# Performance work log

Hardware: AMD Instinct MI355X
Metric: run time of the kernel (lower is better)

## Reference

```python
import jax, jax.numpy as jnp
import numpy as np

B, S, H, SSZ, IN = 1024, 100, 128, 100, 2


def _gru(x, h, Wih, Whh, bih, bhh):
    # PyTorch GRU cell: gates ordered (reset, update, new)
    gx = x @ Wih.T + bih
    gh = h @ Whh.T + bhh
    xr, xz, xn = jnp.split(gx, 3, axis=-1)
    hr, hz, hn = jnp.split(gh, 3, axis=-1)
    r = jax.nn.sigmoid(xr + hr)
    z = jax.nn.sigmoid(xz + hz)
    n = jnp.tanh(xn + r * hn)
    return (1.0 - z) * n + z * h


def _attn(inst_h, rnn_out, W, v):
    # inst_h: [B,S,H], rnn_out: [B,H] -> softmax attention weights [B,S]
    h = jnp.concatenate([inst_h, jnp.broadcast_to(rnn_out[:, None, :], inst_h.shape)], axis=-1)
    s = jax.nn.relu(jnp.einsum('bsk,kh->bsh', h, W)) @ v
    return jax.nn.softmax(s, axis=1)


def setup_inputs() -> dict:
    key = jax.random.key(0)
    k = jax.random.split(key, 32)
    p = lambda i, shape, sc=0.05: sc * jax.random.normal(k[i], shape, jnp.float32)
    instance = jax.random.uniform(k[0], (B, S, IN), jnp.float32)
    # solutions must be per-row permutations of node indices
    solution_1 = jnp.argsort(jax.random.uniform(k[1], (B, S)), axis=1).astype(jnp.int32)
    solution_2 = jnp.argsort(jax.random.uniform(k[2], (B, S)), axis=1).astype(jnp.int32)
    eps = jax.random.normal(k[3], (B, SSZ), jnp.float32)
    return dict(
        instance=instance, solution_1=solution_1, solution_2=solution_2, eps=eps,
        emb_i_W=p(4, (H, IN)), emb_i_b=jnp.zeros(H, jnp.float32),
        emb_r_W=p(5, (H, IN)), emb_r_b=jnp.zeros(H, jnp.float32),
        attn_W=p(6, (2 * H, H)), attn_v=p(7, (H,)),
        gru_Wih=p(8, (3 * H, H)), gru_Whh=p(9, (3 * H, H)),
        gru_bih=jnp.zeros(3 * H, jnp.float32), gru_bhh=jnp.zeros(3 * H, jnp.float32),
        grud_Wih=p(10, (3 * H, 2 * H)), grud_Whh=p(11, (3 * H, H)),
        grud_bih=jnp.zeros(3 * H, jnp.float32), grud_bhh=jnp.zeros(3 * H, jnp.float32),
        enc_fc1_W=p(12, (SSZ, H)), enc_fc1_b=jnp.zeros(SSZ, jnp.float32),
        enc_fc2_W=p(13, (SSZ, H)), enc_fc2_b=jnp.zeros(SSZ, jnp.float32),
        ptr_W=p(14, (2 * H, H)), ptr_v=p(15, (H,)),
        pfc1_W=p(16, (2 * H, 2 * H + SSZ)), pfc1_b=jnp.zeros(2 * H, jnp.float32),
        pfc2_W=p(17, (H, 2 * H)), pfc2_b=jnp.zeros(H, jnp.float32),
    )


def reference(instance, solution_1, solution_2, eps,
              emb_i_W, emb_i_b, emb_r_W, emb_r_b, attn_W, attn_v,
              gru_Wih, gru_Whh, gru_bih, gru_bhh,
              grud_Wih, grud_Whh, grud_bih, grud_bhh,
              enc_fc1_W, enc_fc1_b, enc_fc2_W, enc_fc2_b,
              ptr_W, ptr_v, pfc1_W, pfc1_b, pfc2_W, pfc2_b):
    b_idx = jnp.arange(B)
    inst_h = instance @ emb_i_W.T + emb_i_b  # [B,S,H]
    emb_r = lambda x: x @ emb_r_W.T + emb_r_b
    take = lambda ptr: instance[b_idx, ptr]  # gather node coords [B,IN]

    # ---------------- Encoder ----------------
    def enc_step(carry, ptr):
        h1, h2, ref_h = carry
        h1 = _gru(ref_h, h1, gru_Wih, gru_Whh, gru_bih, gru_bhh)
        a = _attn(inst_h, h1, attn_W, attn_v)
        context = jnp.einsum('bs,bsh->bh', a, inst_h)
        ref_h = emb_r(take(ptr))
        rnn_in = jnp.concatenate([ref_h, context], axis=-1)  # [B,2H]
        h2 = _gru(rnn_in, h2, grud_Wih, grud_Whh, grud_bih, grud_bhh)
        return (h1, h2, ref_h), None

    z0 = jnp.zeros((B, H), instance.dtype)
    ref_h0 = emb_r(take(solution_1[:, 0]))
    (_, h2, _), _ = jax.lax.scan(enc_step, (z0, z0, ref_h0), solution_1[:, 1:].T)
    mu = h2 @ enc_fc1_W.T + enc_fc1_b
    log_var = h2 @ enc_fc2_W.T + enc_fc2_b
    Z = mu + eps * jnp.exp(0.5 * log_var)

    # ---------------- Decoder (teacher forcing) ----------------
    mask0 = jnp.ones((B, S), instance.dtype).at[b_idx, solution_2[:, 0]].set(0.0)

    def dec_step(carry, ptr):
        h1, ref_in, mask = carry
        ref_h = emb_r(ref_in)
        h1 = _gru(ref_h, h1, gru_Wih, gru_Whh, gru_bih, gru_bhh)
        a = _attn(inst_h, h1, attn_W, attn_v)
        context = jnp.einsum('bs,bsh->bh', a, inst_h)
        fc_in = jnp.concatenate([context, Z, ref_h], axis=-1)  # [B, 2H+SSZ]
        fc_out = (fc_in @ pfc1_W.T + pfc1_b) @ pfc2_W.T + pfc2_b  # no activation, as in torch
        hcat = jnp.concatenate([inst_h, jnp.broadcast_to(fc_out[:, None, :], inst_h.shape)], axis=-1)
        logits = jnp.tanh(jnp.einsum('bsk,kh->bsh', hcat, ptr_W)) @ ptr_v  # [B,S]
        probs = jax.nn.softmax(logits + jnp.log(mask), axis=1)
        logp = jnp.log(probs[b_idx, ptr])
        pred = jnp.argmax(probs, axis=1)
        mask = mask.at[b_idx, ptr].set(0.0)  # tsp.update_mask: mark chosen node visited
        return (h1, take(ptr), mask), (pred, logp)

    init = (z0, take(solution_2[:, 0]), mask0)
    _, (preds, logps) = jax.lax.scan(dec_step, init, solution_2[:, 1:].T)
    tour_idx = jnp.concatenate([solution_2[:, :1], preds.T.astype(solution_2.dtype)], axis=1)
    tour_logp = logps.T  # [B, S-1]
    return (mu, log_var, Z, tour_idx, tour_logp)
```

## Files before the change

### kernel.cpp

```cpp
#include <hip/hip_runtime.h>
#include <math.h>

static constexpr int NB  = 1024;
static constexpr int NS  = 100;
static constexpr int NH  = 128;
static constexpr int GPB = 2;
static constexpr int NTHR = 256;
static constexpr int NBLK = NB / GPB;

static constexpr int OUT_MU = 0;
static constexpr int OUT_LV = NB * NS;
static constexpr int OUT_Z  = 2 * NB * NS;
static constexpr int OUT_TI = 3 * NB * NS;
static constexpr int OUT_LP = 4 * NB * NS;

#define NEGF (-3.4e38f)

template<int C4>
__device__ __forceinline__ void dot2x3f(const float* __restrict__ wr0,
        const float* __restrict__ wr1, const float* __restrict__ wr2,
        const float* __restrict__ x0, const float* __restrict__ x1,
        float& r00, float& r01, float& r10, float& r11, float& r20, float& r21)
{
    const float4* W0 = reinterpret_cast<const float4*>(wr0);
    const float4* W1 = reinterpret_cast<const float4*>(wr1);
    const float4* W2 = reinterpret_cast<const float4*>(wr2);
    const float4* X0 = reinterpret_cast<const float4*>(x0);
    const float4* X1 = reinterpret_cast<const float4*>(x1);
    float a00 = 0.f, a01 = 0.f, a10 = 0.f, a11 = 0.f, a20 = 0.f, a21 = 0.f;
    #pragma unroll 8
    for (int c = 0; c < C4; ++c) {
        float4 u0 = W0[c], u1 = W1[c], u2 = W2[c];
        float4 v0 = X0[c], v1 = X1[c];
        a00 = fmaf(u0.x, v0.x, a00); a00 = fmaf(u0.y, v0.y, a00); a00 = fmaf(u0.z, v0.z, a00); a00 = fmaf(u0.w, v0.w, a00);
        a01 = fmaf(u0.x, v1.x, a01); a01 = fmaf(u0.y, v1.y, a01); a01 = fmaf(u0.z, v1.z, a01); a01 = fmaf(u0.w, v1.w, a01);
        a10 = fmaf(u1.x, v0.x, a10); a10 = fmaf(u1.y, v0.y, a10); a10 = fmaf(u1.z, v0.z, a10); a10 = fmaf(u1.w, v0.w, a10);
        a11 = fmaf(u1.x, v1.x, a11); a11 = fmaf(u1.y, v1.y, a11); a11 = fmaf(u1.z, v1.z, a11); a11 = fmaf(u1.w, v1.w, a11);
        a20 = fmaf(u2.x, v0.x, a20); a20 = fmaf(u2.y, v0.y, a20); a20 = fmaf(u2.z, v0.z, a20); a20 = fmaf(u2.w, v0.w, a20);
        a21 = fmaf(u2.x, v1.x, a21); a21 = fmaf(u2.y, v1.y, a21); a21 = fmaf(u2.z, v1.z, a21); a21 = fmaf(u2.w, v1.w, a21);
    }
    r00 = a00; r01 = a01; r10 = a10; r11 = a11; r20 = a20; r21 = a21;
}

template<int C4>
__device__ __forceinline__ void dot2f(const float* __restrict__ w,
        const float* __restrict__ x0, const float* __restrict__ x1, float& r0, float& r1)
{
    const float4* W = reinterpret_cast<const float4*>(w);
    const float4* X0 = reinterpret_cast<const float4*>(x0);
    const float4* X1 = reinterpret_cast<const float4*>(x1);
    float a0 = 0.f, a1 = 0.f;
    #pragma unroll 8
    for (int c = 0; c < C4; ++c) {
        float4 u = W[c];
        float4 v0 = X0[c], v1 = X1[c];
        a0 = fmaf(u.x, v0.x, a0); a0 = fmaf(u.y, v0.y, a0); a0 = fmaf(u.z, v0.z, a0); a0 = fmaf(u.w, v0.w, a0);
        a1 = fmaf(u.x, v1.x, a1); a1 = fmaf(u.y, v1.y, a1); a1 = fmaf(u.z, v1.z, a1); a1 = fmaf(u.w, v1.w, a1);
    }
    r0 = a0; r1 = a1;
}

template<int C4>
__device__ __forceinline__ void dot1f(const float* __restrict__ w,
        const float* __restrict__ x0, float& r0)
{
    const float4* W = reinterpret_cast<const float4*>(w);
    const float4* X0 = reinterpret_cast<const float4*>(x0);
    float a0 = 0.f;
    #pragma unroll 8
    for (int c = 0; c < C4; ++c) {
        float4 u = W[c];
        float4 v0 = X0[c];
        a0 = fmaf(u.x, v0.x, a0); a0 = fmaf(u.y, v0.y, a0); a0 = fmaf(u.z, v0.z, a0); a0 = fmaf(u.w, v0.w, a0);
    }
    r0 = a0;
}

template<int C4>
__device__ __forceinline__ double dotwd(const float* __restrict__ w, const float* __restrict__ x)
{
    const float4* W = reinterpret_cast<const float4*>(w);
    double a = 0.0;
    #pragma unroll 8
    for (int c = 0; c < C4; ++c) {
        float4 u = W[c];
        const float* p = x + 4 * c;
        a = fma((double)u.x, (double)p[0], a);
        a = fma((double)u.y, (double)p[1], a);
        a = fma((double)u.z, (double)p[2], a);
        a = fma((double)u.w, (double)p[3], a);
    }
    return a;
}

__device__ __forceinline__ void gruc(const float* __restrict__ bih, const float* __restrict__ bhh,
        const float* __restrict__ pa, const float* __restrict__ pb, float* __restrict__ h, int j)
{
    double r = 1.0 / (1.0 + exp(-(((double)pa[j]        + (double)bih[j])        + ((double)pb[j]        + (double)bhh[j]))));
    double z = 1.0 / (1.0 + exp(-(((double)pa[NH + j]   + (double)bih[NH + j])   + ((double)pb[NH + j]   + (double)bhh[NH + j]))));
    double n = tanh(((double)pa[2*NH + j] + (double)bih[2*NH + j]) + r * ((double)pb[2*NH + j] + (double)bhh[2*NH + j]));
    h[j] = (float)((1.0 - z) * n + z * (double)h[j]);
}

__global__ __launch_bounds__(NTHR) void vae_v14(
    const float* __restrict__ instance, const int* __restrict__ sol1,
    const int* __restrict__ sol2, const float* __restrict__ eps,
    const float* __restrict__ emb_i_W, const float* __restrict__ emb_i_b,
    const float* __restrict__ emb_r_W, const float* __restrict__ emb_r_b,
    const float* __restrict__ attn_W, const float* __restrict__ attn_v,
    const float* __restrict__ gru_Wih, const float* __restrict__ gru_Whh,
    const float* __restrict__ gru_bih, const float* __restrict__ gru_bhh,
    const float* __restrict__ grud_Wih, const float* __restrict__ grud_Whh,
    const float* __restrict__ grud_bih, const float* __restrict__ grud_bhh,
    const float* __restrict__ efc1_W, const float* __restrict__ efc1_b,
    const float* __restrict__ efc2_W, const float* __restrict__ efc2_b,
    const float* __restrict__ ptr_W, const float* __restrict__ ptr_v,
    const float* __restrict__ pfc1_W, const float* __restrict__ pfc1_b,
    const float* __restrict__ pfc2_W, const float* __restrict__ pfc2_b,
    float* __restrict__ out)
{
    __shared__ float  s_x[GPB][360];
    __shared__ float  s_h1[GPB][NH], s_h2[GPB][NH], s_fco[GPB][NH];
    __shared__ float  s_fch[GPB][256];
    __shared__ float  s_pa[GPB][3 * NH], s_pb[GPB][3 * NH];
    __shared__ double s_qh[GPB][NH];
    __shared__ double s_qpA[GPB][NH], s_qpB[GPB][NH];
    __shared__ double2 dAa[NH], dAp[NH];
    __shared__ double dAba[NH], dAbp[NH];
    __shared__ float  s_lg[GPB][NS], s_a[GPB][NS];
    __shared__ float  s_c0[GPB][NS], s_c1[GPB][NS], s_msk[GPB][NS];
    __shared__ float  t_wi0[NH], t_wi1[NH], t_bi[NH];
    __shared__ float  t_wr0[NH], t_wr1[NH], t_br[NH];
    __shared__ float  t_va[NH], t_vp[NH];
    __shared__ float  t_gbih[3*NH], t_gbhh[3*NH], t_dbih[3*NH], t_dbhh[3*NH];
    __shared__ float  t_p1b[256], t_p2b[NH];
    __shared__ int    s_sol1[GPB][NS], s_sol2[GPB][NS];
    __shared__ float  s_red[GPB][2];
    __shared__ double s_redd[GPB][2];
    __shared__ int    s_ri[GPB][2];
    __shared__ float  s_rc0[GPB], s_rc1[GPB];

    const int tid = threadIdx.x;
    const int bbase = blockIdx.x * GPB;
    const int j = tid & (NH - 1);
    const int half = tid >> 7;
    const int g = half;
    const int lane = tid & 63;
    const int wid = (tid >> 6) & 1;

    if (tid < NH) {
        t_wi0[tid] = emb_i_W[2*tid]; t_wi1[tid] = emb_i_W[2*tid+1]; t_bi[tid] = emb_i_b[tid];
        t_wr0[tid] = emb_r_W[2*tid]; t_wr1[tid] = emb_r_W[2*tid+1]; t_br[tid] = emb_r_b[tid];
        t_va[tid] = attn_v[tid]; t_vp[tid] = ptr_v[tid];
        t_p2b[tid] = pfc2_b[tid];
    }
    t_p1b[tid] = pfc1_b[tid];
    for (int i = tid; i < 3 * NH; i += NTHR) {
        t_gbih[i] = gru_bih[i]; t_gbhh[i] = gru_bhh[i];
        t_dbih[i] = grud_bih[i]; t_dbhh[i] = grud_bhh[i];
    }
    for (int i = tid; i < GPB * NS; i += NTHR) {
        int gg = i / NS, s = i - gg * NS;
        s_c0[gg][s] = instance[(size_t)((bbase + gg) * NS + s) * 2 + 0];
        s_c1[gg][s] = instance[(size_t)((bbase + gg) * NS + s) * 2 + 1];
        s_sol1[gg][s] = sol1[(bbase + gg) * NS + s];
        s_sol2[gg][s] = sol2[(bbase + gg) * NS + s];
    }
    s_h1[g][j] = 0.f;
    s_h2[g][j] = 0.f;
    __syncthreads();
    {
        const float* Wm = (half == 0) ? attn_W : ptr_W;
        double a0 = 0.0, a1 = 0.0, ab = 0.0;
        for (int k = 0; k < NH; ++k) {
            double wv = (double)Wm[(size_t)k * NH + j];
            a0 = fma((double)t_wi0[k], wv, a0);
            a1 = fma((double)t_wi1[k], wv, a1);
            ab = fma((double)t_bi[k],  wv, ab);
        }
        if (half == 0) { dAa[j].x = a0; dAa[j].y = a1; dAba[j] = ab; }
        else           { dAp[j].x = a0; dAp[j].y = a1; dAbp[j] = ab; }
    }
    {
        int sp = s_sol1[g][0];
        s_x[g][j] = fmaf(s_c0[g][sp], t_wr0[j], fmaf(s_c1[g][sp], t_wr1[j], t_br[j]));
    }
    __syncthreads();

    for (int t = 1; t < NS; ++t) {
        if (half == 0) {
            float a00,a01,a10,a11,a20,a21;
            dot2x3f<32>(gru_Wih + (size_t)j * NH, gru_Wih + (size_t)(NH + j) * NH,
                        gru_Wih + (size_t)(2*NH + j) * NH, s_x[0], s_x[1],
                        a00,a01,a10,a11,a20,a21);
            s_pa[0][j] = a00;        s_pa[1][j] = a01;
            s_pa[0][NH + j] = a10;   s_pa[1][NH + j] = a11;
            s_pa[0][2*NH + j] = a20; s_pa[1][2*NH + j] = a21;
        } else {
            float a00,a01,a10,a11,a20,a21;
            dot2x3f<32>(gru_Whh + (size_t)j * NH, gru_Whh + (size_t)(NH + j) * NH,
                        gru_Whh + (size_t)(2*NH + j) * NH, s_h1[0], s_h1[1],
                        a00,a01,a10,a11,a20,a21);
            s_pb[0][j] = a00;        s_pb[1][j] = a01;
            s_pb[0][NH + j] = a10;   s_pb[1][NH + j] = a11;
            s_pb[0][2*NH + j] = a20; s_pb[1][2*NH + j] = a21;
        }
        __syncthreads();
        gruc(t_gbih, t_gbhh, s_pa[g], s_pb[g], s_h1[g], j);
        __syncthreads();
        {
            const float* col = attn_W + (size_t)NH * NH + j;
            const int k0 = half * 64;
            double a00=0.0,a01=0.0,a02=0.0,a03=0.0;
            double a10=0.0,a11=0.0,a12=0.0,a13=0.0;
            #pragma unroll 8
            for (int k = 0; k < 64; k += 4) {
                float w0 = col[(size_t)(k0+k+0) * NH];
                float w1 = col[(size_t)(k0+k+1) * NH];
                float w2 = col[(size_t)(k0+k+2) * NH];
                float w3 = col[(size_t)(k0+k+3) * NH];
                float4 h0 = *reinterpret_cast<const float4*>(&s_h1[0][k0+k]);
                float4 h1v = *reinterpret_cast<const float4*>(&s_h1[1][k0+k]);
                a00 = fma((double)w0, (double)h0.x, a00);
                a01 = fma((double)w1, (double)h0.y, a01);
                a02 = fma((double)w2, (double)h0.z, a02);
                a03 = fma((double)w3, (double)h0.w, a03);
                a10 = fma((double)w0, (double)h1v.x, a10);
                a11 = fma((double)w1, (double)h1v.y, a11);
                a12 = fma((double)w2, (double)h1v.z, a12);
                a13 = fma((double)w3, (double)h1v.w, a13);
            }
            if (half == 0) { s_qpA[0][j] = (a00+a01)+(a02+a03); s_qpA[1][j] = (a10+a11)+(a12+a13); }
            else           { s_qpB[0][j] = (a00+a01)+(a02+a03); s_qpB[1][j] = (a10+a11)+(a12+a13); }
        }
        __syncthreads();
        s_qh[g][j] = dAba[j] + (s_qpA[g][j] + s_qpB[g][j]);
        __syncthreads();
        if (j < NS) {
            double c00 = (double)s_c0[g][j], c10 = (double)s_c1[g][j];
            double acc0 = 0.0, acc1 = 0.0, acc2 = 0.0, acc3 = 0.0;
            #pragma unroll 4
            for (int h = 0; h < NH; h += 4) {
                double2 A0 = dAa[h+0], A1 = dAa[h+1], A2 = dAa[h+2], A3 = dAa[h+3];
                double p0 = fma(c00, A0.x, fma(c10, A0.y, s_qh[g][h+0]));
                double p1 = fma(c00, A1.x, fma(c10, A1.y, s_qh[g][h+1]));
                double p2 = fma(c00, A2.x, fma(c10, A2.y, s_qh[g][h+2]));
                double p3 = fma(c00, A3.x, fma(c10, A3.y, s_qh[g][h+3]));
                acc0 = fma(fmax(p0, 0.0), (double)t_va[h+0], acc0);
                acc1 = fma(fmax(p1, 0.0), (double)t_va[h+1], acc1);
                acc2 = fma(fmax(p2, 0.0), (double)t_va[h+2], acc2);
                acc3 = fma(fmax(p3, 0.0), (double)t_va[h+3], acc3);
            }
            s_lg[g][j] = (float)(((acc0 + acc1) + (acc2 + acc3)));
        }
        __syncthreads();
        {
            float a = s_lg[g][lane];
            float b = (lane + 64 < NS) ? s_lg[g][lane + 64] : NEGF;
            float m = fmaxf(a, b);
            m = fmaxf(m, __shfl_xor(m, 32)); m = fmaxf(m, __shfl_xor(m, 16));
            m = fmaxf(m, __shfl_xor(m, 8));  m = fmaxf(m, __shfl_xor(m, 4));
            m = fmaxf(m, __shfl_xor(m, 2));  m = fmaxf(m, __shfl_xor(m, 1));
            float fv = 0.f;
            if (j < NS) { fv = (float)exp((double)s_lg[g][j] - (double)m); s_a[g][j] = fv; }
            double ps = (double)fv;
            ps += __shfl_xor(ps, 32); ps += __shfl_xor(ps, 16);
            ps += __shfl_xor(ps, 8);  ps += __shfl_xor(ps, 4);
            ps += __shfl_xor(ps, 2);  ps += __shfl_xor(ps, 1);
            if (lane == 0) s_redd[g][wid] = ps;
        }
        __syncthreads();
        if (j < NS) {
            double se = s_redd[g][0] + s_redd[g][1];
            s_a[g][j] = (float)((double)s_a[g][j] / se);
        }
        __syncthreads();
        {
            float w0 = t_wi0[j], w1 = t_wi1[j], bb = t_bi[j];
            double a0 = 0.0, a1 = 0.0, a2 = 0.0, a3 = 0.0;
            #pragma unroll 5
            for (int s = 0; s < NS; s += 4) {
                float ih0 = fmaf(s_c0[g][s+0], w0, fmaf(s_c1[g][s+0], w1, bb));
                float ih1 = fmaf(s_c0[g][s+1], w0, fmaf(s_c1[g][s+1], w1, bb));
                float ih2 = fmaf(s_c0[g][s+2], w0, fmaf(s_c1[g][s+2], w1, bb));
                float ih3 = fmaf(s_c0[g][s+3], w0, fmaf(s_c1[g][s+3], w1, bb));
                a0 += (double)s_a[g][s+0] * (double)ih0;
                a1 += (double)s_a[g][s+1] * (double)ih1;
                a2 += (double)s_a[g][s+2] * (double)ih2;
                a3 += (double)s_a[g][s+3] * (double)ih3;
            }
            s_x[g][NH + j] = (float)(((a0 + a1) + (a2 + a3)));
            int sp = s_sol1[g][t];
            s_x[g][j] = fmaf(s_c0[g][sp], t_wr0[j], fmaf(s_c1[g][sp], t_wr1[j], t_br[j]));
        }
        __syncthreads();
        if (half == 0) {
            float a00,a01,a10,a11,a20,a21;
            dot2x3f<64>(grud_Wih + (size_t)j * 256, grud_Wih + (size_t)(NH + j) * 256,
                        grud_Wih + (size_t)(2*NH + j) * 256, s_x[0], s_x[1],
                        a00,a01,a10,a11,a20,a21);
            s_pa[0][j] = a00;        s_pa[1][j] = a01;
            s_pa[0][NH + j] = a10;   s_pa[1][NH + j] = a11;
            s_pa[0][2*NH + j] = a20; s_pa[1][2*NH + j] = a21;
        } else {
            float a00,a01,a10,a11,a20,a21;
            dot2x3f<32>(grud_Whh + (size_t)j * NH, grud_Whh + (size_t)(NH + j) * NH,
                        grud_Whh + (size_t)(2*NH + j) * NH, s_h2[0], s_h2[1],
                        a00,a01,a10,a11,a20,a21);
            s_pb[0][j] = a00;        s_pb[1][j] = a01;
            s_pb[0][NH + j] = a10;   s_pb[1][NH + j] = a11;
            s_pb[0][2*NH + j] = a20; s_pb[1][2*NH + j] = a21;
        }
        __syncthreads();
        gruc(t_dbih, t_dbhh, s_pa[g], s_pb[g], s_h2[g], j);
        __syncthreads();
    }

    for (int idx = tid; idx < GPB * NS; idx += NTHR) {
        int gg = idx / NS, s = idx - gg * NS, b = bbase + gg;
        double mu = dotwd<32>(efc1_W + (size_t)s * NH, s_h2[gg]) + (double)efc1_b[s];
        double lv = dotwd<32>(efc2_W + (size_t)s * NH, s_h2[gg]) + (double)efc2_b[s];
        double z  = mu + (double)eps[(size_t)b * NS + s] * exp(0.5 * lv);
        out[OUT_MU + b * NS + s] = (float)mu;
        out[OUT_LV + b * NS + s] = (float)lv;
        out[OUT_Z  + b * NS + s] = (float)z;
        s_x[gg][NH + s] = (float)z;
    }
    for (int i = tid; i < GPB * NS; i += NTHR) {
        int gg = i / NS, s = i - gg * NS;
        s_msk[gg][s] = 1.f;
    }
    s_h1[g][j] = 0.f;
    __syncthreads();
    if (tid < GPB) {
        int b = bbase + tid;
        int s0 = s_sol2[tid][0];
        s_msk[tid][s0] = 0.f;
        s_rc0[tid] = s_c0[tid][s0];
        s_rc1[tid] = s_c1[tid][s0];
        out[OUT_TI + b * NS + 0] = (float)s0;
    }
    __syncthreads();

    for (int t = 1; t < NS; ++t) {
        s_x[g][228 + j] = fmaf(s_rc0[g], t_wr0[j], fmaf(s_rc1[g], t_wr1[j], t_br[j]));
        __syncthreads();
        if (half == 0) {
            float a00,a01,a10,a11,a20,a21;
            dot2x3f<32>(gru_Wih + (size_t)j * NH, gru_Wih + (size_t)(NH + j) * NH,
                        gru_Wih + (size_t)(2*NH + j) * NH, s_x[0]+228, s_x[1]+228,
                        a00,a01,a10,a11,a20,a21);
            s_pa[0][j] = a00;        s_pa[1][j] = a01;
            s_pa[0][NH + j] = a10;   s_pa[1][NH + j] = a11;
            s_pa[0][2*NH + j] = a20; s_pa[1][2*NH + j] = a21;
        } else {
            float a00,a01,a10,a11,a20,a21;
            dot2x3f<32>(gru_Whh + (size_t)j * NH, gru_Whh + (size_t)(NH + j) * NH,
                        gru_Whh + (size_t)(2*NH + j) * NH, s_h1[0], s_h1[1],
                        a00,a01,a10,a11,a20,a21);
            s_pb[0][j] = a00;        s_pb[1][j] = a01;
            s_pb[0][NH + j] = a10;   s_pb[1][NH + j] = a11;
            s_pb[0][2*NH + j] = a20; s_pb[1][2*NH + j] = a21;
        }
        __syncthreads();
        gruc(t_gbih, t_gbhh, s_pa[g], s_pb[g], s_h1[g], j);
        __syncthreads();
        {
            const float* col = attn_W + (size_t)NH * NH + j;
            const int k0 = half * 64;
            double a00=0.0,a01=0.0,a02=0.0,a03=0.0;
            double a10=0.0,a11=0.0,a12=0.0,a13=0.0;
            #pragma unroll 8
            for (int k = 0; k < 64; k += 4) {
                float w0 = col[(size_t)(k0+k+0) * NH];
                float w1 = col[(size_t)(k0+k+1) * NH];
                float w2 = col[(size_t)(k0+k+2) * NH];
                float w3 = col[(size_t)(k0+k+3) * NH];
                float4 h0 = *reinterpret_cast<const float4*>(&s_h1[0][k0+k]);
                float4 h1v = *reinterpret_cast<const float4*>(&s_h1[1][k0+k]);
                a00 = fma((double)w0, (double)h0.x, a00);
                a01 = fma((double)w1, (double)h0.y, a01);
                a02 = fma((double)w2, (double)h0.z, a02);
                a03 = fma((double)w3, (double)h0.w, a03);
                a10 = fma((double)w0, (double)h1v.x, a10);
                a11 = fma((double)w1, (double)h1v.y, a11);
                a12 = fma((double)w2, (double)h1v.z, a12);
                a13 = fma((double)w3, (double)h1v.w, a13);
            }
            if (half == 0) { s_qpA[0][j] = (a00+a01)+(a02+a03); s_qpA[1][j] = (a10+a11)+(a12+a13); }
            else           { s_qpB[0][j] = (a00+a01)+(a02+a03); s_qpB[1][j] = (a10+a11)+(a12+a13); }
        }
        __syncthreads();
        s_qh[g][j] = dAba[j] + (s_qpA[g][j] + s_qpB[g][j]);
        __syncthreads();
        if (j < NS) {
            double c00 = (double)s_c0[g][j], c10 = (double)s_c1[g][j];
            double acc0 = 0.0, acc1 = 0.0, acc2 = 0.0, acc3 = 0.0;
            #pragma unroll 4
            for (int h = 0; h < NH; h += 4) {
                double2 A0 = dAa[h+0], A1 = dAa[h+1], A2 = dAa[h+2], A3 = dAa[h+3];
                double p0 = fma(c00, A0.x, fma(c10, A0.y, s_qh[g][h+0]));
                double p1 = fma(c00, A1.x, fma(c10, A1.y, s_qh[g][h+1]));
                double p2 = fma(c00, A2.x, fma(c10, A2.y, s_qh[g][h+2]));
                double p3 = fma(c00, A3.x, fma(c10, A3.y, s_qh[g][h+3]));
                acc0 = fma(fmax(p0, 0.0), (double)t_va[h+0], acc0);
                acc1 = fma(fmax(p1, 0.0), (double)t_va[h+1], acc1);
                acc2 = fma(fmax(p2, 0.0), (double)t_va[h+2], acc2);
                acc3 = fma(fmax(p3, 0.0), (double)t_va[h+3], acc3);
            }
            s_lg[g][j] = (float)(((acc0 + acc1) + (acc2 + acc3)));
        }
        __syncthreads();
        {
            float a = s_lg[g][lane];
            float b = (lane + 64 < NS) ? s_lg[g][lane + 64] : NEGF;
            float m = fmaxf(a, b);
            m = fmaxf(m, __shfl_xor(m, 32)); m = fmaxf(m, __shfl_xor(m, 16));
            m = fmaxf(m, __shfl_xor(m, 8));  m = fmaxf(m, __shfl_xor(m, 4));
            m = fmaxf(m, __shfl_xor(m, 2));  m = fmaxf(m, __shfl_xor(m, 1));
            float fv = 0.f;
            if (j < NS) { fv = (float)exp((double)s_lg[g][j] - (double)m); s_a[g][j] = fv; }
            double ps = (double)fv;
            ps += __shfl_xor(ps, 32); ps += __shfl_xor(ps, 16);
            ps += __shfl_xor(ps, 8);  ps += __shfl_xor(ps, 4);
            ps += __shfl_xor(ps, 2);  ps += __shfl_xor(ps, 1);
            if (lane == 0) s_redd[g][wid] = ps;
        }
        __syncthreads();
        if (j < NS) {
            double se = s_redd[g][0] + s_redd[g][1];
            s_a[g][j] = (float)((double)s_a[g][j] / se);
        }
        __syncthreads();
        {
            float w0 = t_wi0[j], w1 = t_wi1[j], bb = t_bi[j];
            double a0 = 0.0, a1 = 0.0, a2 = 0.0, a3 = 0.0;
            #pragma unroll 5
            for (int s = 0; s < NS; s += 4) {
                float ih0 = fmaf(s_c0[g][s+0], w0, fmaf(s_c1[g][s+0], w1, bb));
                float ih1 = fmaf(s_c0[g][s+1], w0, fmaf(s_c1[g][s+1], w1, bb));
                float ih2 = fmaf(s_c0[g][s+2], w0, fmaf(s_c1[g][s+2], w1, bb));
                float ih3 = fmaf(s_c0[g][s+3], w0, fmaf(s_c1[g][s+3], w1, bb));
                a0 += (double)s_a[g][s+0] * (double)ih0;
                a1 += (double)s_a[g][s+1] * (double)ih1;
                a2 += (double)s_a[g][s+2] * (double)ih2;
                a3 += (double)s_a[g][s+3] * (double)ih3;
            }
            s_x[g][j] = (float)(((a0 + a1) + (a2 + a3)));
        }
        __syncthreads();
        {
            float r0, r1;
            dot2f<89>(pfc1_W + (size_t)tid * 356, s_x[0], s_x[1], r0, r1);
            float bb = t_p1b[tid];
            s_fch[0][tid] = r0 + bb; s_fch[1][tid] = r1 + bb;
        }
        __syncthreads();
        {
            float r0;
            dot1f<64>(pfc2_W + (size_t)j * 256, s_fch[g], r0);
            s_fco[g][j] = r0 + t_p2b[j];
        }
        __syncthreads();
        {
            const float* col = ptr_W + (size_t)NH * NH + j;
            const int k0 = half * 64;
            double a00=0.0,a01=0.0,a02=0.0,a03=0.0;
            double a10=0.0,a11=0.0,a12=0.0,a13=0.0;
            #pragma unroll 8
            for (int k = 0; k < 64; k += 4) {
                float w0 = col[(size_t)(k0+k+0) * NH];
                float w1 = col[(size_t)(k0+k+1) * NH];
                float w2 = col[(size_t)(k0+k+2) * NH];
                float w3 = col[(size_t)(k0+k+3) * NH];
                float4 f0 = *reinterpret_cast<const float4*>(&s_fco[0][k0+k]);
                float4 f1 = *reinterpret_cast<const float4*>(&s_fco[1][k0+k]);
                a00 = fma((double)w0, (double)f0.x, a00);
                a01 = fma((double)w1, (double)f0.y, a01);
                a02 = fma((double)w2, (double)f0.z, a02);
                a03 = fma((double)w3, (double)f0.w, a03);
                a10 = fma((double)w0, (double)f1.x, a10);
                a11 = fma((double)w1, (double)f1.y, a11);
                a12 = fma((double)w2, (double)f1.z, a12);
                a13 = fma((double)w3, (double)f1.w, a13);
            }
            if (half == 0) { s_qpA[0][j] = (a00+a01)+(a02+a03); s_qpA[1][j] = (a10+a11)+(a12+a13); }
            else           { s_qpB[0][j] = (a00+a01)+(a02+a03); s_qpB[1][j] = (a10+a11)+(a12+a13); }
        }
        __syncthreads();
        s_qh[g][j] = dAbp[j] + (s_qpA[g][j] + s_qpB[g][j]);
        __syncthreads();
        if (j < NS) {
            double c00 = (double)s_c0[g][j], c10 = (double)s_c1[g][j];
            double acc0 = 0.0, acc1 = 0.0, acc2 = 0.0, acc3 = 0.0;
            #pragma unroll 4
            for (int h = 0; h < NH; h += 4) {
                double2 A0 = dAp[h+0], A1 = dAp[h+1], A2 = dAp[h+2], A3 = dAp[h+3];
                double p0 = fma(c00, A0.x, fma(c10, A0.y, s_qh[g][h+0]));
                double p1 = fma(c00, A1.x, fma(c10, A1.y, s_qh[g][h+1]));
                double p2 = fma(c00, A2.x, fma(c10, A2.y, s_qh[g][h+2]));
                double p3 = fma(c00, A3.x, fma(c10, A3.y, s_qh[g][h+3]));
                acc0 = fma((double)tanhf((float)p0), (double)t_vp[h+0], acc0);
                acc1 = fma((double)tanhf((float)p1), (double)t_vp[h+1], acc1);
                acc2 = fma((double)tanhf((float)p2), (double)t_vp[h+2], acc2);
                acc3 = fma((double)tanhf((float)p3), (double)t_vp[h+3], acc3);
            }
            s_lg[g][j] = (float)(((acc0 + acc1) + (acc2 + acc3)));
        }
        __syncthreads();
        {
            float la = s_lg[g][lane];
            float ma = (s_msk[g][lane] > 0.f) ? la : NEGF;
            float lb = NEGF;
            if (lane + 64 < NS) lb = (s_msk[g][lane + 64] > 0.f) ? s_lg[g][lane + 64] : NEGF;
            float m = fmaxf(ma, lb);
            m = fmaxf(m, __shfl_xor(m, 32)); m = fmaxf(m, __shfl_xor(m, 16));
            m = fmaxf(m, __shfl_xor(m, 8));  m = fmaxf(m, __shfl_xor(m, 4));
            m = fmaxf(m, __shfl_xor(m, 2));  m = fmaxf(m, __shfl_xor(m, 1));
            float fv = 0.f;
            if (j < NS) {
                fv = (s_msk[g][j] > 0.f) ? (float)exp((double)s_lg[g][j] - (double)m) : 0.f;
                s_a[g][j] = fv;
            }
            float  bv = (j < NS) ? fv : -1.f;
            int    bi = (j < NS) ? j  : NS;
            double ps = (j < NS) ? (double)fv : 0.0;
            #pragma unroll
            for (int o = 32; o >= 1; o >>= 1) {
                float  ov = __shfl_xor(bv, o);
                int    oi = __shfl_xor(bi, o);
                double op = __shfl_xor(ps, o);
                ps += op;
                if (ov > bv || (ov == bv && oi < bi)) { bv = ov; bi = oi; }
            }
            if (lane == 0) { s_red[g][wid] = bv; s_ri[g][wid] = bi; s_redd[g][wid] = ps; }
        }
        __syncthreads();
        if (tid < GPB) {
            int gg = tid, b = bbase + gg;
            float m = -1.f; int mi = NS; double se = 0.0;
            for (int i = 0; i < 2; ++i) {
                se += s_redd[gg][i];
                float v = s_red[gg][i]; int vi = s_ri[gg][i];
                if (v > m || (v == m && vi < mi)) { m = v; mi = vi; }
            }
            int pt = s_sol2[gg][t];
            double logp = log((double)s_a[gg][pt] / se);
            out[OUT_TI + b * NS + t]             = (float)mi;
            out[OUT_LP + b * (NS - 1) + (t - 1)] = (float)logp;
            s_msk[gg][pt] = 0.f;
            s_rc0[gg] = s_c0[gg][pt];
            s_rc1[gg] = s_c1[gg][pt];
        }
        __syncthreads();
    }
}

extern "C" void kernel_launch(void* const* d_in, const int* in_sizes, int n_in,
                              void* d_out, int out_size, void* d_ws, size_t ws_size,
                              hipStream_t stream)
{
    (void)in_sizes; (void)n_in; (void)out_size; (void)d_ws; (void)ws_size;
    vae_v14<<<NBLK, NTHR, 0, stream>>>(
        (const float*)d_in[0], (const int*)d_in[1], (const int*)d_in[2], (const float*)d_in[3],
        (const float*)d_in[4], (const float*)d_in[5], (const float*)d_in[6], (const float*)d_in[7],
        (const float*)d_in[8], (const float*)d_in[9], (const float*)d_in[10], (const float*)d_in[11],
        (const float*)d_in[12], (const float*)d_in[13], (const float*)d_in[14], (const float*)d_in[15],
        (const float*)d_in[16], (const float*)d_in[17], (const float*)d_in[18], (const float*)d_in[19],
        (const float*)d_in[20], (const float*)d_in[21], (const float*)d_in[22], (const float*)d_in[23],
        (const float*)d_in[24], (const float*)d_in[25], (const float*)d_in[26], (const float*)d_in[27],
        (float*)d_out);
}
```

Baseline: 12.26 ms.

## Keep attention/pointer query weight columns in registers and rebalance decoder GRU gate work

Preloads each thread's 64-element slices of the hidden-part columns of attn_W and ptr_W into register arrays once, so the per-step query projections no longer re-read those columns from global memory. The decoder GRU's six gate dot products are split evenly across both thread halves (three each) instead of all input gates on one half and all hidden gates on the other, which removes the imbalance from the 256-wide input rows. Launch bounds now request two blocks per CU and the dot-product unroll is reduced to limit register pressure. The 128 extra registers per thread risk spills or lower occupancy.

```diff
diff --git a/kernel.cpp b/kernel.cpp
--- a/kernel.cpp
+++ b/kernel.cpp
@@ -28,7 +28,7 @@
     const float4* X0 = reinterpret_cast<const float4*>(x0);
     const float4* X1 = reinterpret_cast<const float4*>(x1);
     float a00 = 0.f, a01 = 0.f, a10 = 0.f, a11 = 0.f, a20 = 0.f, a21 = 0.f;
-    #pragma unroll 8
+    #pragma unroll 4
     for (int c = 0; c < C4; ++c) {
         float4 u0 = W0[c], u1 = W1[c], u2 = W2[c];
         float4 v0 = X0[c], v1 = X1[c];
@@ -102,7 +102,7 @@
     h[j] = (float)((1.0 - z) * n + z * (double)h[j]);
 }
 
-__global__ __launch_bounds__(NTHR) void vae_v14(
+__global__ __launch_bounds__(NTHR, 2) void vae_v17(
     const float* __restrict__ instance, const int* __restrict__ sol1,
     const int* __restrict__ sol2, const float* __restrict__ eps,
     const float* __restrict__ emb_i_W, const float* __restrict__ emb_i_b,
@@ -147,6 +147,7 @@
     const int g = half;
     const int lane = tid & 63;
     const int wid = (tid >> 6) & 1;
+    const int k0 = half * 64;
 
     if (tid < NH) {
         t_wi0[tid] = emb_i_W[2*tid]; t_wi1[tid] = emb_i_W[2*tid+1]; t_bi[tid] = emb_i_b[tid];
@@ -168,15 +169,26 @@
     }
     s_h1[g][j] = 0.f;
     s_h2[g][j] = 0.f;
+
+    float wqa[64], wqp[64];
+    {
+        const float* colA = attn_W + (size_t)NH * NH + j;
+        const float* colP = ptr_W  + (size_t)NH * NH + j;
+        #pragma unroll
+        for (int k = 0; k < 64; ++k) {
+            wqa[k] = colA[(size_t)(k0 + k) * NH];
+            wqp[k] = colP[(size_t)(k0 + k) * NH];
+        }
+    }
     __syncthreads();
     {
         const float* Wm = (half == 0) ? attn_W : ptr_W;
         double a0 = 0.0, a1 = 0.0, ab = 0.0;
         for (int k = 0; k < NH; ++k) {
-            double wv = (double)Wm[(size_t)k * NH + j];
-            a0 = fma((double)t_wi0[k], wv, a0);
-            a1 = fma((double)t_wi1[k], wv, a1);
-            ab = fma((double)t_bi[k],  wv, ab);
+            double wv2 = (double)Wm[(size_t)k * NH + j];
+            a0 = fma((double)t_wi0[k], wv2, a0);
+            a1 = fma((double)t_wi1[k], wv2, a1);
+            ab = fma((double)t_bi[k],  wv2, ab);
         }
         if (half == 0) { dAa[j].x = a0; dAa[j].y = a1; dAba[j] = ab; }
         else           { dAp[j].x = a0; dAp[j].y = a1; dAbp[j] = ab; }
@@ -209,26 +221,21 @@
         gruc(t_gbih, t_gbhh, s_pa[g], s_pb[g], s_h1[g], j);
         __syncthreads();
         {
-            const float* col = attn_W + (size_t)NH * NH + j;
-            const int k0 = half * 64;
             double a00=0.0,a01=0.0,a02=0.0,a03=0.0;
             double a10=0.0,a11=0.0,a12=0.0,a13=0.0;
-            #pragma unroll 8
-            for (int k = 0; k < 64; k += 4) {
-                float w0 = col[(size_t)(k0+k+0) * NH];
-                float w1 = col[(size_t)(k0+k+1) * NH];
-                float w2 = col[(size_t)(k0+k+2) * NH];
-                float w3 = col[(size_t)(k0+k+3) * NH];
+            #pragma unroll
+            for (int k4 = 0; k4 < 16; ++k4) {
+                const int k = 4 * k4;
                 float4 h0 = *reinterpret_cast<const float4*>(&s_h1[0][k0+k]);
                 float4 h1v = *reinterpret_cast<const float4*>(&s_h1[1][k0+k]);
-                a00 = fma((double)w0, (double)h0.x, a00);
-                a01 = fma((double)w1, (double)h0.y, a01);
-                a02 = fma((double)w2, (double)h0.z, a02);
-                a03 = fma((double)w3, (double)h0.w, a03);
-                a10 = fma((double)w0, (double)h1v.x, a10);
-                a11 = fma((double)w1, (double)h1v.y, a11);
-                a12 = fma((double)w2, (double)h1v.z, a12);
-                a13 = fma((double)w3, (double)h1v.w, a13);
+                a00 = fma((double)wqa[k+0], (double)h0.x, a00);
+                a01 = fma((double)wqa[k+1], (double)h0.y, a01);
+                a02 = fma((double)wqa[k+2], (double)h0.z, a02);
+                a03 = fma((double)wqa[k+3], (double)h0.w, a03);
+                a10 = fma((double)wqa[k+0], (double)h1v.x, a10);
+                a11 = fma((double)wqa[k+1], (double)h1v.y, a11);
+                a12 = fma((double)wqa[k+2], (double)h1v.z, a12);
+                a13 = fma((double)wqa[k+3], (double)h1v.w, a13);
             }
             if (half == 0) { s_qpA[0][j] = (a00+a01)+(a02+a03); s_qpA[1][j] = (a10+a11)+(a12+a13); }
             else           { s_qpB[0][j] = (a00+a01)+(a02+a03); s_qpB[1][j] = (a10+a11)+(a12+a13); }
@@ -294,22 +301,24 @@
             s_x[g][j] = fmaf(s_c0[g][sp], t_wr0[j], fmaf(s_c1[g][sp], t_wr1[j], t_br[j]));
         }
         __syncthreads();
-        if (half == 0) {
-            float a00,a01,a10,a11,a20,a21;
-            dot2x3f<64>(grud_Wih + (size_t)j * 256, grud_Wih + (size_t)(NH + j) * 256,
-                        grud_Wih + (size_t)(2*NH + j) * 256, s_x[0], s_x[1],
-                        a00,a01,a10,a11,a20,a21);
-            s_pa[0][j] = a00;        s_pa[1][j] = a01;
-            s_pa[0][NH + j] = a10;   s_pa[1][NH + j] = a11;
-            s_pa[0][2*NH + j] = a20; s_pa[1][2*NH + j] = a21;
-        } else {
-            float a00,a01,a10,a11,a20,a21;
-            dot2x3f<32>(grud_Whh + (size_t)j * NH, grud_Whh + (size_t)(NH + j) * NH,
-                        grud_Whh + (size_t)(2*NH + j) * NH, s_h2[0], s_h2[1],
-                        a00,a01,a10,a11,a20,a21);
-            s_pb[0][j] = a00;        s_pb[1][j] = a01;
-            s_pb[0][NH + j] = a10;   s_pb[1][NH + j] = a11;
-            s_pb[0][2*NH + j] = a20; s_pb[1][2*NH + j] = a21;
+        {
+            if (half == 0) {
+                float r0, r1;
+                dot2f<64>(grud_Wih + (size_t)j * 256, s_x[0], s_x[1], r0, r1);
+                s_pa[0][j] = r0; s_pa[1][j] = r1;
+                dot2f<64>(grud_Wih + (size_t)(NH + j) * 256, s_x[0], s_x[1], r0, r1);
+                s_pa[0][NH + j] = r0; s_pa[1][NH + j] = r1;
+                dot2f<32>(grud_Whh + (size_t)(2*NH + j) * NH, s_h2[0], s_h2[1], r0, r1);
+                s_pb[0][2*NH + j] = r0; s_pb[1][2*NH + j] = r1;
+            } else {
+                float r0, r1;
+                dot2f<64>(grud_Wih + (size_t)(2*NH + j) * 256, s_x[0], s_x[1], r0, r1);
+                s_pa[0][2*NH + j] = r0; s_pa[1][2*NH + j] = r1;
+                dot2f<32>(grud_Whh + (size_t)j * NH, s_h2[0], s_h2[1], r0, r1);
+                s_pb[0][j] = r0; s_pb[1][j] = r1;
+                dot2f<32>(grud_Whh + (size_t)(NH + j) * NH, s_h2[0], s_h2[1], r0, r1);
+                s_pb[0][NH + j] = r0; s_pb[1][NH + j] = r1;
+            }
         }
         __syncthreads();
         gruc(t_dbih, t_dbhh, s_pa[g], s_pb[g], s_h2[g], j);
@@ -366,26 +375,21 @@
         gruc(t_gbih, t_gbhh, s_pa[g], s_pb[g], s_h1[g], j);
         __syncthreads();
         {
-            const float* col = attn_W + (size_t)NH * NH + j;
-            const int k0 = half * 64;
             double a00=0.0,a01=0.0,a02=0.0,a03=0.0;
             double a10=0.0,a11=0.0,a12=0.0,a13=0.0;
-            #pragma unroll 8
-            for (int k = 0; k < 64; k += 4) {
-                float w0 = col[(size_t)(k0+k+0) * NH];
-                float w1 = col[(size_t)(k0+k+1) * NH];
-                float w2 = col[(size_t)(k0+k+2) * NH];
-                float w3 = col[(size_t)(k0+k+3) * NH];
+            #pragma unroll
+            for (int k4 = 0; k4 < 16; ++k4) {
+                const int k = 4 * k4;
                 float4 h0 = *reinterpret_cast<const float4*>(&s_h1[0][k0+k]);
                 float4 h1v = *reinterpret_cast<const float4*>(&s_h1[1][k0+k]);
-                a00 = fma((double)w0, (double)h0.x, a00);
-                a01 = fma((double)w1, (double)h0.y, a01);
-                a02 = fma((double)w2, (double)h0.z, a02);
-                a03 = fma((double)w3, (double)h0.w, a03);
-                a10 = fma((double)w0, (double)h1v.x, a10);
-                a11 = fma((double)w1, (double)h1v.y, a11);
-                a12 = fma((double)w2, (double)h1v.z, a12);
-                a13 = fma((double)w3, (double)h1v.w, a13);
+                a00 = fma((double)wqa[k+0], (double)h0.x, a00);
+                a01 = fma((double)wqa[k+1], (double)h0.y, a01);
+                a02 = fma((double)wqa[k+2], (double)h0.z, a02);
+                a03 = fma((double)wqa[k+3], (double)h0.w, a03);
+                a10 = fma((double)wqa[k+0], (double)h1v.x, a10);
+                a11 = fma((double)wqa[k+1], (double)h1v.y, a11);
+                a12 = fma((double)wqa[k+2], (double)h1v.z, a12);
+                a13 = fma((double)wqa[k+3], (double)h1v.w, a13);
             }
             if (half == 0) { s_qpA[0][j] = (a00+a01)+(a02+a03); s_qpA[1][j] = (a10+a11)+(a12+a13); }
             else           { s_qpB[0][j] = (a00+a01)+(a02+a03); s_qpB[1][j] = (a10+a11)+(a12+a13); }
@@ -463,26 +467,21 @@
         }
         __syncthreads();
         {
-            const float* col = ptr_W + (size_t)NH * NH + j;
-            const int k0 = half * 64;
             double a00=0.0,a01=0.0,a02=0.0,a03=0.0;
             double a10=0.0,a11=0.0,a12=0.0,a13=0.0;
-            #pragma unroll 8
-            for (int k = 0; k < 64; k += 4) {
-                float w0 = col[(size_t)(k0+k+0) * NH];
-                float w1 = col[(size_t)(k0+k+1) * NH];
-                float w2 = col[(size_t)(k0+k+2) * NH];
-                float w3 = col[(size_t)(k0+k+3) * NH];
+            #pragma unroll
+            for (int k4 = 0; k4 < 16; ++k4) {
+                const int k = 4 * k4;
                 float4 f0 = *reinterpret_cast<const float4*>(&s_fco[0][k0+k]);
                 float4 f1 = *reinterpret_cast<const float4*>(&s_fco[1][k0+k]);
-                a00 = fma((double)w0, (double)f0.x, a00);
-                a01 = fma((double)w1, (double)f0.y, a01);
-                a02 = fma((double)w2, (double)f0.z, a02);
-                a03 = fma((double)w3, (double)f0.w, a03);
-                a10 = fma((double)w0, (double)f1.x, a10);
-                a11 = fma((double)w1, (double)f1.y, a11);
-                a12 = fma((double)w2, (double)f1.z, a12);
-                a13 = fma((double)w3, (double)f1.w, a13);
+                a00 = fma((double)wqp[k+0], (double)f0.x, a00);
+                a01 = fma((double)wqp[k+1], (double)f0.y, a01);
+                a02 = fma((double)wqp[k+2], (double)f0.z, a02);
+                a03 = fma((double)wqp[k+3], (double)f0.w, a03);
+                a10 = fma((double)wqp[k+0], (double)f1.x, a10);
+                a11 = fma((double)wqp[k+1], (double)f1.y, a11);
+                a12 = fma((double)wqp[k+2], (double)f1.z, a12);
+                a13 = fma((double)wqp[k+3], (double)f1.w, a13);
             }
             if (half == 0) { s_qpA[0][j] = (a00+a01)+(a02+a03); s_qpA[1][j] = (a10+a11)+(a12+a13); }
             else           { s_qpB[0][j] = (a00+a01)+(a02+a03); s_qpB[1][j] = (a10+a11)+(a12+a13); }
@@ -561,7 +560,7 @@
                               hipStream_t stream)
 {
     (void)in_sizes; (void)n_in; (void)out_size; (void)d_ws; (void)ws_size;
-    vae_v14<<<NBLK, NTHR, 0, stream>>>(
+    vae_v17<<<NBLK, NTHR, 0, stream>>>(
         (const float*)d_in[0], (const int*)d_in[1], (const int*)d_in[2], (const float*)d_in[3],
         (const float*)d_in[4], (const float*)d_in[5], (const float*)d_in[6], (const float*)d_in[7],
         (const float*)d_in[8], (const float*)d_in[9], (const float*)d_in[10], (const float*)d_in[11],
```

Result: slower. 15.52 ms (+26.6%).
